# Performance work log

Hardware: AMD Instinct MI355X
Metric: run time of the kernel (lower is better)

## Reference

```python
import jax, jax.numpy as jnp
import numpy as np

D = 512
EPS = 1e-5  # torch BatchNorm1d default eps


def swish(x):
    return x * jax.nn.sigmoid(x)


def batchnorm_train(x, gamma, beta):
    # BatchNorm1d in training mode: biased batch stats
    m = jnp.mean(x, axis=0)
    v = jnp.mean((x - m) ** 2, axis=0)
    return gamma * (x - m) / jnp.sqrt(v + EPS) + beta


def setup_inputs() -> dict:
    key = jax.random.key(0)
    k_fea, k_w1, k_w2, k_lerp = jax.random.split(key, 4)
    bs, P = 32768, 8192
    fea = jax.random.normal(k_fea, (bs, D), dtype=jnp.float32)
    # first P rows are the minority (positive) class
    lbl = jnp.concatenate([jnp.ones((P, 1), jnp.int32), jnp.zeros((bs - P, 1), jnp.int32)], axis=0)
    scale = 1.0 / np.sqrt(D)
    W1 = jax.random.normal(k_w1, (D, D), dtype=jnp.float32) * scale
    W2 = jax.random.normal(k_w2, (D, D), dtype=jnp.float32) * scale
    b1 = jnp.zeros((D,), jnp.float32)
    b2 = jnp.zeros((D,), jnp.float32)
    g1 = jnp.ones((D,), jnp.float32)
    g2 = jnp.ones((D,), jnp.float32)
    beta1 = jnp.zeros((D,), jnp.float32)
    beta2 = jnp.zeros((D,), jnp.float32)
    lerp_w = jax.random.uniform(k_lerp, (P, 3), dtype=jnp.float32)
    return dict(fea=fea, lbl=lbl, W1=W1, b1=b1, g1=g1, beta1=beta1,
                W2=W2, b2=b2, g2=g2, beta2=beta2, lerp_w=lerp_w, num_pos=P)


def reference(fea, lbl, W1, b1, g1, beta1, W2, b2, g2, beta2, lerp_w, num_pos):
    # fea_transform: Linear -> BN -> Swish -> Linear -> BN -> Swish
    h = swish(batchnorm_train(fea @ W1 + b1, g1, beta1))
    h = swish(batchnorm_train(h @ W2 + b2, g2, beta2))

    # SMOTE path (training mode): KNN over positive-class features
    pos_idx = jnp.nonzero(lbl[:, 0] > 0, size=num_pos)[0]  # static-size gather
    x = h[pos_idx]                                          # (P, D)
    sq = jnp.sum(x * x, axis=-1)                            # (P,)
    # negative squared pairwise distance; topk largest == nearest
    neg_dist = 2.0 * (x @ x.T) - sq[:, None] - sq[None, :]  # (P, P)
    _, idx = jax.lax.top_k(neg_dist, 3)                     # (P, 3), idx[:,0] == self

    a = x[idx[:, 0]]                                        # (P, D) anchor
    b = x[idx]                                              # (P, 3, D) neighbors
    # torch.lerp(a, b, w) = a + w * (b - a), one random w per (i, j)
    new_fea = a[:, None, :] + lerp_w[..., None] * (b - a[:, None, :])
    new_fea = new_fea.reshape(-1, D)                        # (3P, D), row-major matches i,j loop order

    fea_out = jnp.concatenate([h, new_fea], axis=0)
    lbl_out = jnp.concatenate([lbl, jnp.ones((new_fea.shape[0], 1), lbl.dtype)], axis=0)
    return fea_out, lbl_out
```

## Files before the change

kernel.cpp:

```cpp
#include <hip/hip_runtime.h>
#include <math.h>

#define NEG_INF -3.402823466e38f
#define NSPLIT 16

typedef __attribute__((ext_vector_type(8))) short bf16x8;
typedef __attribute__((ext_vector_type(4))) float f32x4;

__device__ __forceinline__ void gload_lds16(const unsigned short* g, unsigned short* l) {
  __builtin_amdgcn_global_load_lds(
      (const __attribute__((address_space(1))) unsigned int*)g,
      (__attribute__((address_space(3))) unsigned int*)l, 16, 0, 0);
}
__device__ __forceinline__ void gload_lds16f(const float* g, float* l) {
  __builtin_amdgcn_global_load_lds(
      (const __attribute__((address_space(1))) unsigned int*)g,
      (__attribute__((address_space(3))) unsigned int*)l, 16, 0, 0);
}

__device__ __forceinline__ unsigned short f2bf(float f) {
  union { float f; unsigned int u; } a; a.f = f;
  unsigned int u = a.u;
  return (unsigned short)((u + 0x7fffu + ((u >> 16) & 1u)) >> 16);
}

__device__ __forceinline__ void split3_8(f32x4 a, f32x4 b,
                                         bf16x8& hi, bf16x8& md, bf16x8& lo) {
  union { bf16x8 v; unsigned int u[4]; } H, M, L;
  float f[8];
  f[0]=a[0]; f[1]=a[1]; f[2]=a[2]; f[3]=a[3];
  f[4]=b[0]; f[5]=b[1]; f[6]=b[2]; f[7]=b[3];
#pragma unroll
  for (int p = 0; p < 4; ++p) {
    union { float f; unsigned int u; } x0, x1, h0, h1, r0, r1, m0, m1, s0, s1;
    x0.f = f[2*p]; x1.f = f[2*p+1];
    H.u[p] = (x0.u >> 16) | (x1.u & 0xffff0000u);
    h0.u = x0.u & 0xffff0000u; h1.u = x1.u & 0xffff0000u;
    r0.f = x0.f - h0.f;        r1.f = x1.f - h1.f;
    M.u[p] = (r0.u >> 16) | (r1.u & 0xffff0000u);
    m0.u = r0.u & 0xffff0000u; m1.u = r1.u & 0xffff0000u;
    s0.f = r0.f - m0.f;        s1.f = r1.f - m1.f;
    L.u[p] = (s0.u >> 16) | (s1.u & 0xffff0000u);
  }
  hi = H.v; md = M.v; lo = L.v;
}

__global__ __launch_bounds__(256) void split_w_t3(const float* __restrict__ W,
    unsigned short* __restrict__ Th, unsigned short* __restrict__ Tm,
    unsigned short* __restrict__ Tl)
{
  __shared__ float T[64][65];
  int k0 = blockIdx.x * 64, n0 = blockIdx.y * 64;
  int tid = threadIdx.x;
  int r = tid >> 4, c4 = (tid & 15) << 2;
#pragma unroll
  for (int p = 0; p < 4; ++p) {
    int row = r + p * 16;
    float4 v = *(const float4*)&W[(size_t)(k0 + row) * 512 + n0 + c4];
    T[c4 + 0][row] = v.x; T[c4 + 1][row] = v.y;
    T[c4 + 2][row] = v.z; T[c4 + 3][row] = v.w;
  }
  __syncthreads();
  int nr = tid >> 2, kc = (tid & 3) << 4;
#pragma unroll
  for (int u = 0; u < 16; ++u) {
    union { float f; unsigned int u; } x, h, rr, m, ss;
    x.f = T[nr][kc + u];
    unsigned short hb = (unsigned short)(x.u >> 16);
    h.u = x.u & 0xffff0000u;
    rr.f = x.f - h.f;
    unsigned short mb = (unsigned short)(rr.u >> 16);
    m.u = rr.u & 0xffff0000u;
    ss.f = rr.f - m.f;
    unsigned short lb = (unsigned short)(ss.u >> 16);
    size_t o = (size_t)(n0 + nr) * 512 + k0 + kc + u;
    Th[o] = hb; Tm[o] = mb; Tl[o] = lb;
  }
}

__global__ __launch_bounds__(256, 2) void gemm_split3(
    const float* __restrict__ A, const unsigned short* __restrict__ Bth,
    const unsigned short* __restrict__ Btm, const unsigned short* __restrict__ Btl,
    const float* __restrict__ bias, float* __restrict__ C, float* __restrict__ partial)
{
  __shared__ char smem[81920];
  const int tid = threadIdx.x;
  const int w = tid >> 6, lane = tid & 63;
  const int wr = w >> 1, wc = w & 1;
  const int bm = blockIdx.x * 128, bn = blockIdx.y * 128;
  const int fr = lane & 15, fg = lane >> 4;
  const int arow = tid >> 3, acb = (tid & 7) << 4;
  const int brow = tid >> 2, bcb = (tid & 3) << 4;

  f32x4 acc[4][4];
#pragma unroll
  for (int mi = 0; mi < 4; ++mi)
#pragma unroll
    for (int ni = 0; ni < 4; ++ni) acc[mi][ni] = (f32x4){0.f, 0.f, 0.f, 0.f};

  auto STAGE = [&](int buf, int ktf) {
    float* sA = (float*)(smem + buf * 40960);
    unsigned short* sBh = (unsigned short*)(smem + buf * 40960 + 16384);
    unsigned short* sBm = sBh + 4096;
    unsigned short* sBl = sBm + 4096;
#pragma unroll
    for (int p = 0; p < 4; ++p) {
      int row = arow + p * 32;
      int cb = acb ^ ((row & 7) << 4);
      gload_lds16f(&A[(size_t)(bm + row) * 512 + ktf + (cb >> 2)],
                   &sA[row * 32 + (acb >> 2)]);
    }
#pragma unroll
    for (int p = 0; p < 2; ++p) {
      int row = brow + p * 64;
      int cb = bcb ^ (((row >> 1) & 3) << 4);
      int so = row * 32 + (bcb >> 1);
      gload_lds16(&Bth[(size_t)(bn + row) * 512 + ktf + (cb >> 1)], &sBh[so]);
      gload_lds16(&Btm[(size_t)(bn + row) * 512 + ktf + (cb >> 1)], &sBm[so]);
      gload_lds16(&Btl[(size_t)(bn + row) * 512 + ktf + (cb >> 1)], &sBl[so]);
    }
  };

  STAGE(0, 0);
  __syncthreads();
  for (int it = 0; it < 16; ++it) {
    int cur = it & 1;
    if (it + 1 < 16) STAGE(cur ^ 1, (it + 1) * 32);
    float* sA = (float*)(smem + cur * 40960);
    unsigned short* sBh = (unsigned short*)(smem + cur * 40960 + 16384);
    unsigned short* sBm = sBh + 4096;
    unsigned short* sBl = sBm + 4096;
    bf16x8 bh[4], bmf[4], blf[4];
#pragma unroll
    for (int ni = 0; ni < 4; ++ni) {
      int row = wc * 64 + ni * 16 + fr;
      int off = row * 32 + (((fg * 16) ^ (((row >> 1) & 3) << 4)) >> 1);
      bh[ni]  = *(const bf16x8*)&sBh[off];
      bmf[ni] = *(const bf16x8*)&sBm[off];
      blf[ni] = *(const bf16x8*)&sBl[off];
    }
    bf16x8 ah[4], am[4], al[4];
#pragma unroll
    for (int mi = 0; mi < 4; ++mi) {
      int row = wr * 64 + mi * 16 + fr;
      int swz = (row & 7) << 4;
      const char* rb = (const char*)(sA + row * 32);
      f32x4 f0 = *(const f32x4*)(rb + ((fg * 32) ^ swz));
      f32x4 f1 = *(const f32x4*)(rb + ((fg * 32 + 16) ^ swz));
      split3_8(f0, f1, ah[mi], am[mi], al[mi]);
    }
#pragma unroll
    for (int mi = 0; mi < 4; ++mi)
#pragma unroll
      for (int ni = 0; ni < 4; ++ni) {
        acc[mi][ni] = __builtin_amdgcn_mfma_f32_16x16x32_bf16(al[mi], bh[ni],  acc[mi][ni], 0, 0, 0);
        acc[mi][ni] = __builtin_amdgcn_mfma_f32_16x16x32_bf16(am[mi], bmf[ni], acc[mi][ni], 0, 0, 0);
        acc[mi][ni] = __builtin_amdgcn_mfma_f32_16x16x32_bf16(ah[mi], blf[ni], acc[mi][ni], 0, 0, 0);
        acc[mi][ni] = __builtin_amdgcn_mfma_f32_16x16x32_bf16(am[mi], bh[ni],  acc[mi][ni], 0, 0, 0);
        acc[mi][ni] = __builtin_amdgcn_mfma_f32_16x16x32_bf16(ah[mi], bmf[ni], acc[mi][ni], 0, 0, 0);
        acc[mi][ni] = __builtin_amdgcn_mfma_f32_16x16x32_bf16(ah[mi], bh[ni],  acc[mi][ni], 0, 0, 0);
      }
    __syncthreads();
  }
  float bno[4], s[4] = {0, 0, 0, 0}, q[4] = {0, 0, 0, 0};
#pragma unroll
  for (int ni = 0; ni < 4; ++ni) bno[ni] = bias[bn + wc * 64 + ni * 16 + fr];
#pragma unroll
  for (int mi = 0; mi < 4; ++mi) {
    int row = bm + wr * 64 + mi * 16 + fg * 4;
#pragma unroll
    for (int ni = 0; ni < 4; ++ni) {
      int col = bn + wc * 64 + ni * 16 + fr;
#pragma unroll
      for (int r = 0; r < 4; ++r) {
        float v = acc[mi][ni][r] + bno[ni];
        C[(size_t)(row + r) * 512 + col] = v;
        s[ni] += v; q[ni] += v * v;
      }
    }
  }
#pragma unroll
  for (int ni = 0; ni < 4; ++ni) {
    float ss = s[ni], qq = q[ni];
    ss += __shfl_xor(ss, 16); ss += __shfl_xor(ss, 32);
    qq += __shfl_xor(qq, 16); qq += __shfl_xor(qq, 32);
    if (fg == 0) {
      int slot = blockIdx.x * 2 + wr;
      int col = bn + wc * 64 + ni * 16 + fr;
      partial[(size_t)(slot * 2 + 0) * 512 + col] = ss;
      partial[(size_t)(slot * 2 + 1) * 512 + col] = qq;
    }
  }
}

__global__ __launch_bounds__(256) void bn_reduce1(
    const float* __restrict__ partial, float* __restrict__ partial2, int nslot)
{
  int g = blockIdx.x, p = blockIdx.y;
  int per = nslot >> 4;
  int t = threadIdx.x;
#pragma unroll
  for (int cc = 0; cc < 2; ++cc) {
    int c = t + cc * 256;
    float s = 0.f;
    for (int s0 = 0; s0 < per; ++s0) {
      int slot = g * per + s0;
      s += partial[(size_t)(slot * 2 + p) * 512 + c];
    }
    partial2[(size_t)(g * 2 + p) * 512 + c] = s;
  }
}

__global__ void bn_finalize(
    const float* __restrict__ partial2, const float* __restrict__ g,
    const float* __restrict__ beta, float* __restrict__ scale,
    float* __restrict__ shift, int rows)
{
  int c = blockIdx.x * blockDim.x + threadIdx.x;
  if (c >= 512) return;
  float s = 0, s2 = 0;
  for (int b = 0; b < 16; ++b) {
    s  += partial2[(size_t)(b * 2 + 0) * 512 + c];
    s2 += partial2[(size_t)(b * 2 + 1) * 512 + c];
  }
  float m = s / rows;
  float v = s2 / rows - m * m;
  if (v < 0) v = 0;
  float sc = g[c] / sqrtf(v + 1e-5f);
  scale[c] = sc;
  shift[c] = beta[c] - m * sc;
}

__global__ void bn_swish(
    const float* __restrict__ Y, const float* __restrict__ scale,
    const float* __restrict__ shift, float* __restrict__ H, int total4)
{
  int i = blockIdx.x * blockDim.x + threadIdx.x;
  if (i >= total4) return;
  float4 y = ((const float4*)Y)[i];
  int c = (i * 4) & 511;
  float z;
  float4 o;
  z = y.x * scale[c + 0] + shift[c + 0]; o.x = z / (1.f + expf(-z));
  z = y.y * scale[c + 1] + shift[c + 1]; o.y = z / (1.f + expf(-z));
  z = y.z * scale[c + 2] + shift[c + 2]; o.z = z / (1.f + expf(-z));
  z = y.w * scale[c + 3] + shift[c + 3]; o.w = z / (1.f + expf(-z));
  ((float4*)H)[i] = o;
}

__global__ __launch_bounds__(1024) void pos_count(const int* __restrict__ lbl, int n,
                                                  int* __restrict__ cnt,
                                                  int* __restrict__ pos, int P)
{
  int b = blockIdx.x, tid = threadIdx.x;
  int i = b * 1024 + tid;
  if (i < P) pos[i] = 0;
  int pred = (i < n) && (lbl[i] > 0);
  unsigned long long m = __ballot(pred);
  __shared__ int ws[16];
  if ((tid & 63) == 0) ws[tid >> 6] = __popcll(m);
  __syncthreads();
  if (tid == 0) { int s = 0; for (int k = 0; k < 16; ++k) s += ws[k]; cnt[b] = s; }
}

__global__ void pos_prefix(int* __restrict__ cnt, int nb)
{
  if (threadIdx.x == 0) {
    int s = 0;
    for (int b = 0; b < nb; ++b) { int c = cnt[b]; cnt[b] = s; s += c; }
  }
}

__global__ __launch_bounds__(1024) void pos_scatter(const int* __restrict__ lbl, int n,
                                                    const int* __restrict__ cntp,
                                                    int* __restrict__ pos, int P)
{
  int b = blockIdx.x, tid = threadIdx.x;
  int i = b * 1024 + tid;
  int pred = (i < n) && (lbl[i] > 0);
  unsigned long long m = __ballot(pred);
  __shared__ int ws[16];
  int wid = tid >> 6, lane = tid & 63;
  if (lane == 0) ws[wid] = __popcll(m);
  __syncthreads();
  int wbase = 0;
  for (int w2 = 0; w2 < wid; ++w2) wbase += ws[w2];
  int rank = cntp[b] + wbase + __popcll(m & ((1ull << lane) - 1ull));
  if (pred && rank < P) pos[rank] = i;
}

__global__ void gather_sq(const float* __restrict__ H, const int* __restrict__ pos,
                          float* __restrict__ X, unsigned short* __restrict__ Xh,
                          float* __restrict__ sq)
{
  int r = blockIdx.x, t = threadIdx.x;
  int src = pos[r];
  float4 v = *(const float4*)&H[src * 512 + t * 4];
  *(float4*)&X[r * 512 + t * 4] = v;
  ushort4 hv;
  hv.x = f2bf(v.x); hv.y = f2bf(v.y); hv.z = f2bf(v.z); hv.w = f2bf(v.w);
  *(ushort4*)&Xh[r * 512 + t * 4] = hv;
  float s = v.x * v.x + v.y * v.y + v.z * v.z + v.w * v.w;
#pragma unroll
  for (int off = 32; off > 0; off >>= 1) s += __shfl_down(s, off);
  __shared__ float red[2];
  if ((t & 63) == 0) red[t >> 6] = s;
  __syncthreads();
  if (t == 0) sq[r] = red[0] + red[1];
}

__global__ __launch_bounds__(256, 2) void gram8(
    const unsigned short* __restrict__ Xh, const float* __restrict__ sq, int P,
    float* __restrict__ p8v, int* __restrict__ p8j)
{
  __shared__ unsigned short Ah[128 * 64];
  __shared__ unsigned short Bh[128 * 64];
  __shared__ float dl[4][64][17];
  __shared__ float sqj_l[128];

  const int tid = threadIdx.x;
  const int w = tid >> 6, lane = tid & 63;
  const int wr = w >> 1, wc = w & 1;
  const int bi = blockIdx.x * 128;
  const int jchunk = P / NSPLIT;
  const int jlo = blockIdx.y * jchunk;

  const int srow = tid >> 3;
  const int scb  = (tid & 7) << 4;
  const int fr = lane & 15, fg = lane >> 4;

  float t[8]; int ji[8];
#pragma unroll
  for (int q = 0; q < 8; ++q) { t[q] = NEG_INF; ji[q] = 0x7fffffff; }

  for (int jt = 0; jt < jchunk; jt += 128) {
    const int j0 = jlo + jt;
    if (tid < 128) sqj_l[tid] = sq[j0 + tid];
    f32x4 acc[4][4];
#pragma unroll
    for (int mi = 0; mi < 4; ++mi)
#pragma unroll
      for (int ni = 0; ni < 4; ++ni) acc[mi][ni] = (f32x4){0.f, 0.f, 0.f, 0.f};

    for (int kt = 0; kt < 512; kt += 64) {
#pragma unroll
      for (int it = 0; it < 4; ++it) {
        int row = srow + it * 32;
        int cb = scb ^ ((row & 7) << 4);
        gload_lds16(&Xh[(size_t)(bi + row) * 512 + kt + (cb >> 1)],
                    &Ah[row * 64 + (scb >> 1)]);
        gload_lds16(&Xh[(size_t)(j0 + row) * 512 + kt + (cb >> 1)],
                    &Bh[row * 64 + (scb >> 1)]);
      }
      __syncthreads();
#pragma unroll
      for (int ks = 0; ks < 2; ++ks) {
        bf16x8 af[4], bfr[4];
        int kb = ks * 64 + fg * 16;
#pragma unroll
        for (int mi = 0; mi < 4; ++mi) {
          int row = wr * 64 + mi * 16 + fr;
          af[mi] = *(const bf16x8*)&Ah[row * 64 + ((kb ^ ((row & 7) << 4)) >> 1)];
        }
#pragma unroll
        for (int ni = 0; ni < 4; ++ni) {
          int row = wc * 64 + ni * 16 + fr;
          bfr[ni] = *(const bf16x8*)&Bh[row * 64 + ((kb ^ ((row & 7) << 4)) >> 1)];
        }
#pragma unroll
        for (int mi = 0; mi < 4; ++mi)
#pragma unroll
          for (int ni = 0; ni < 4; ++ni)
            acc[mi][ni] = __builtin_amdgcn_mfma_f32_16x16x32_bf16(
                af[mi], bfr[ni], acc[mi][ni], 0, 0, 0);
      }
      __syncthreads();
    }

#pragma unroll
    for (int qn = 0; qn < 4; ++qn) {
      float sqv = sqj_l[wc * 64 + qn * 16 + fr];
#pragma unroll
      for (int mi = 0; mi < 4; ++mi)
#pragma unroll
        for (int r = 0; r < 4; ++r)
          dl[w][mi * 16 + fg * 4 + r][fr] = 2.0f * acc[mi][qn][r] - sqv;
      __syncthreads();
      int jbase = j0 + wc * 64 + qn * 16;
      for (int c = 0; c < 16; ++c) {
        float v = dl[w][lane][c];
        if (v > t[7]) {
          t[7] = v; ji[7] = jbase + c;
#pragma unroll
          for (int q = 7; q > 0; --q) {
            if (t[q] > t[q - 1]) {
              float tv = t[q]; t[q] = t[q - 1]; t[q - 1] = tv;
              int tj = ji[q]; ji[q] = ji[q - 1]; ji[q - 1] = tj;
            }
          }
        }
      }
      __syncthreads();
    }
  }

  int row = bi + wr * 64 + lane;
  int set = blockIdx.y * 2 + wc;
  size_t base = ((size_t)row * (NSPLIT * 2) + set) * 8;
#pragma unroll
  for (int q = 0; q < 8; ++q) { p8v[base + q] = t[q]; p8j[base + q] = ji[q]; }
}

__global__ void merge8(const float* __restrict__ p8v, const int* __restrict__ p8j,
                       int* __restrict__ cand, int P)
{
  int i = blockIdx.x * blockDim.x + threadIdx.x;
  if (i >= P) return;
  const int S = NSPLIT * 2;
  int head[S];
#pragma unroll
  for (int s = 0; s < S; ++s) head[s] = 0;
  const float* v = p8v + (size_t)i * S * 8;
  const int* j = p8j + (size_t)i * S * 8;
  for (int k = 0; k < 8; ++k) {
    float bv = NEG_INF; int bj = 0x7fffffff; int bs = 0;
#pragma unroll
    for (int s = 0; s < S; ++s) {
      if (head[s] < 8) {
        float vv = v[s * 8 + head[s]];
        int jj = j[s * 8 + head[s]];
        if (vv > bv || (vv == bv && jj < bj)) { bv = vv; bj = jj; bs = s; }
      }
    }
    head[bs]++;
    cand[i * 8 + k] = bj;
  }
}

__global__ __launch_bounds__(64) void rescore(
    const float* __restrict__ X, const float* __restrict__ sq,
    const int* __restrict__ cand, int* __restrict__ idx3)
{
  int i = blockIdx.x;
  int lane = threadIdx.x;
  f32x4 x0 = *(const f32x4*)&X[(size_t)i * 512 + lane * 8];
  f32x4 x1 = *(const f32x4*)&X[(size_t)i * 512 + lane * 8 + 4];
  float d[8]; int cj[8];
#pragma unroll
  for (int c = 0; c < 8; ++c) {
    int j = cand[i * 8 + c];
    cj[c] = j;
    f32x4 y0 = *(const f32x4*)&X[(size_t)j * 512 + lane * 8];
    f32x4 y1 = *(const f32x4*)&X[(size_t)j * 512 + lane * 8 + 4];
    float p = x0.x * y0.x + x0.y * y0.y + x0.z * y0.z + x0.w * y0.w
            + x1.x * y1.x + x1.y * y1.y + x1.z * y1.z + x1.w * y1.w;
#pragma unroll
    for (int off = 32; off > 0; off >>= 1) p += __shfl_xor(p, off);
    d[c] = 2.0f * p - sq[i] - sq[j];
  }
  if (lane == 0) {
    for (int k = 0; k < 3; ++k) {
      int b = 0;
#pragma unroll
      for (int c = 1; c < 8; ++c)
        if (d[c] > d[b] || (d[c] == d[b] && cj[c] < cj[b])) b = c;
      idx3[i * 3 + k] = cj[b];
      d[b] = NEG_INF; cj[b] = 0x7fffffff;
    }
  }
}

__global__ void make_newfea(const float* __restrict__ X, const int* __restrict__ idx3,
                            const float* __restrict__ lw, float* __restrict__ out)
{
  int r = blockIdx.x;
  int i = r / 3, k = r - i * 3;
  int ai = idx3[i * 3 + 0];
  int bi = idx3[i * 3 + k];
  float w = lw[r];
  int t = threadIdx.x;
  float4 av = *(const float4*)&X[ai * 512 + t * 4];
  float4 bv = *(const float4*)&X[bi * 512 + t * 4];
  float4 o;
  o.x = av.x + w * (bv.x - av.x);
  o.y = av.y + w * (bv.y - av.y);
  o.z = av.z + w * (bv.z - av.z);
  o.w = av.w + w * (bv.w - av.w);
  *(float4*)&out[(size_t)r * 512 + t * 4] = o;
}

__global__ void write_lbl(const int* __restrict__ lbl, float* __restrict__ out,
                          int n_in, int n_total)
{
  int i = blockIdx.x * blockDim.x + threadIdx.x;
  if (i < n_total) out[i] = (i < n_in) ? (float)lbl[i] : 1.0f;
}

extern "C" void kernel_launch(void* const* d_in, const int* in_sizes, int n_in,
                              void* d_out, int out_size, void* d_ws, size_t ws_size,
                              hipStream_t stream)
{
  const float* fea   = (const float*)d_in[0];
  const int*   lbl   = (const int*)d_in[1];
  const float* W1    = (const float*)d_in[2];
  const float* b1    = (const float*)d_in[3];
  const float* g1    = (const float*)d_in[4];
  const float* beta1 = (const float*)d_in[5];
  const float* W2    = (const float*)d_in[6];
  const float* b2    = (const float*)d_in[7];
  const float* g2    = (const float*)d_in[8];
  const float* beta2 = (const float*)d_in[9];
  const float* lerp_w = (const float*)d_in[10];

  int bs = in_sizes[0] / 512;
  int P  = in_sizes[10] / 3;
  int n_total = bs + 3 * P;

  float* out_f = (float*)d_out;
  float* Hout = out_f;
  float* newfea = out_f + (size_t)bs * 512;
  float* lbl_out = out_f + (size_t)n_total * 512;

  const size_t MB = 1024 * 1024;
  const size_t KB = 1024;
  char* ws = (char*)d_ws;
  float* Y1 = (float*)ws;
  float* X  = (float*)(ws + 64 * MB);
  unsigned short* W1h = (unsigned short*)(ws + 64 * MB);
  unsigned short* W1m = (unsigned short*)(ws + 64 * MB + 512 * KB);
  unsigned short* W1l = (unsigned short*)(ws + 64 * MB + 1024 * KB);
  unsigned short* W2h = (unsigned short*)(ws + 64 * MB + 1536 * KB);
  unsigned short* W2m = (unsigned short*)(ws + 64 * MB + 2048 * KB);
  unsigned short* W2l = (unsigned short*)(ws + 64 * MB + 2560 * KB);
  float* partial = (float*)(ws + 80 * MB);
  float* scale = (float*)(ws + 82 * MB);
  float* shiftv = scale + 512;
  float* sq = shiftv + 512;
  int* pos = (int*)(sq + 8192);
  int* idx3 = pos + 8192;
  int* cnt = idx3 + 3 * 8192;
  float* partial2 = (float*)(ws + 83 * MB);
  unsigned short* Xh = (unsigned short*)ws;
  float* p8v = (float*)(ws + 8 * MB);
  int*   p8j = (int*)(ws + 16 * MB);
  int*   cand = (int*)(ws + 24 * MB);

  dim3 wgrid(8, 8);
  split_w_t3<<<wgrid, 256, 0, stream>>>(W1, W1h, W1m, W1l);
  split_w_t3<<<wgrid, 256, 0, stream>>>(W2, W2h, W2m, W2l);

  dim3 ggrid(bs / 128, 4);
  int nslot = (bs / 128) * 2;
  dim3 rgrid(16, 2);

  gemm_split3<<<ggrid, 256, 0, stream>>>(fea, W1h, W1m, W1l, b1, Y1, partial);
  bn_reduce1<<<rgrid, 256, 0, stream>>>(partial, partial2, nslot);
  bn_finalize<<<2, 256, 0, stream>>>(partial2, g1, beta1, scale, shiftv, bs);
  bn_swish<<<(bs * 512 / 4 + 255) / 256, 256, 0, stream>>>(Y1, scale, shiftv, Y1, bs * 512 / 4);

  gemm_split3<<<ggrid, 256, 0, stream>>>(Y1, W2h, W2m, W2l, b2, Hout, partial);
  bn_reduce1<<<rgrid, 256, 0, stream>>>(partial, partial2, nslot);
  bn_finalize<<<2, 256, 0, stream>>>(partial2, g2, beta2, scale, shiftv, bs);
  bn_swish<<<(bs * 512 / 4 + 255) / 256, 256, 0, stream>>>(Hout, scale, shiftv, Hout, bs * 512 / 4);

  int nb = (bs + 1023) / 1024;
  pos_count<<<nb, 1024, 0, stream>>>(lbl, bs, cnt, pos, P);
  pos_prefix<<<1, 64, 0, stream>>>(cnt, nb);
  pos_scatter<<<nb, 1024, 0, stream>>>(lbl, bs, cnt, pos, P);
  gather_sq<<<P, 128, 0, stream>>>(Hout, pos, X, Xh, sq);

  dim3 gram_grid(P / 128, NSPLIT);
  gram8<<<gram_grid, 256, 0, stream>>>(Xh, sq, P, p8v, p8j);
  merge8<<<(P + 255) / 256, 256, 0, stream>>>(p8v, p8j, cand, P);
  rescore<<<P, 64, 0, stream>>>(X, sq, cand, idx3);

  make_newfea<<<3 * P, 128, 0, stream>>>(X, idx3, lerp_w, newfea);
  write_lbl<<<(n_total + 255) / 256, 256, 0, stream>>>(lbl, lbl_out, bs, n_total);
}
```

Before: 529.7 us.

## Retile split3 GEMM warps, halve gram splits, and merge candidates wave-parallel

Result: faster. 465.2 us (-12.2%).

```diff
diff --git a/kernel.cpp b/kernel.cpp
--- a/kernel.cpp
+++ b/kernel.cpp
@@ -2,7 +2,7 @@
 #include <math.h>
 
 #define NEG_INF -3.402823466e38f
-#define NSPLIT 16
+#define NSPLIT 8
 
 typedef __attribute__((ext_vector_type(8))) short bf16x8;
 typedef __attribute__((ext_vector_type(4))) float f32x4;
@@ -86,17 +86,16 @@
   __shared__ char smem[81920];
   const int tid = threadIdx.x;
   const int w = tid >> 6, lane = tid & 63;
-  const int wr = w >> 1, wc = w & 1;
   const int bm = blockIdx.x * 128, bn = blockIdx.y * 128;
   const int fr = lane & 15, fg = lane >> 4;
   const int arow = tid >> 3, acb = (tid & 7) << 4;
   const int brow = tid >> 2, bcb = (tid & 3) << 4;
 
-  f32x4 acc[4][4];
-#pragma unroll
-  for (int mi = 0; mi < 4; ++mi)
-#pragma unroll
-    for (int ni = 0; ni < 4; ++ni) acc[mi][ni] = (f32x4){0.f, 0.f, 0.f, 0.f};
+  f32x4 acc[2][8];
+#pragma unroll
+  for (int mi = 0; mi < 2; ++mi)
+#pragma unroll
+    for (int ni = 0; ni < 8; ++ni) acc[mi][ni] = (f32x4){0.f, 0.f, 0.f, 0.f};
 
   auto STAGE = [&](int buf, int ktf) {
     float* sA = (float*)(smem + buf * 40960);
@@ -130,19 +129,10 @@
     unsigned short* sBh = (unsigned short*)(smem + cur * 40960 + 16384);
     unsigned short* sBm = sBh + 4096;
     unsigned short* sBl = sBm + 4096;
-    bf16x8 bh[4], bmf[4], blf[4];
-#pragma unroll
-    for (int ni = 0; ni < 4; ++ni) {
-      int row = wc * 64 + ni * 16 + fr;
-      int off = row * 32 + (((fg * 16) ^ (((row >> 1) & 3) << 4)) >> 1);
-      bh[ni]  = *(const bf16x8*)&sBh[off];
-      bmf[ni] = *(const bf16x8*)&sBm[off];
-      blf[ni] = *(const bf16x8*)&sBl[off];
-    }
-    bf16x8 ah[4], am[4], al[4];
-#pragma unroll
-    for (int mi = 0; mi < 4; ++mi) {
-      int row = wr * 64 + mi * 16 + fr;
+    bf16x8 ah[2], am[2], al[2];
+#pragma unroll
+    for (int mi = 0; mi < 2; ++mi) {
+      int row = w * 32 + mi * 16 + fr;
       int swz = (row & 7) << 4;
       const char* rb = (const char*)(sA + row * 32);
       f32x4 f0 = *(const f32x4*)(rb + ((fg * 32) ^ swz));
@@ -150,45 +140,66 @@
       split3_8(f0, f1, ah[mi], am[mi], al[mi]);
     }
 #pragma unroll
-    for (int mi = 0; mi < 4; ++mi)
-#pragma unroll
-      for (int ni = 0; ni < 4; ++ni) {
-        acc[mi][ni] = __builtin_amdgcn_mfma_f32_16x16x32_bf16(al[mi], bh[ni],  acc[mi][ni], 0, 0, 0);
-        acc[mi][ni] = __builtin_amdgcn_mfma_f32_16x16x32_bf16(am[mi], bmf[ni], acc[mi][ni], 0, 0, 0);
-        acc[mi][ni] = __builtin_amdgcn_mfma_f32_16x16x32_bf16(ah[mi], blf[ni], acc[mi][ni], 0, 0, 0);
-        acc[mi][ni] = __builtin_amdgcn_mfma_f32_16x16x32_bf16(am[mi], bh[ni],  acc[mi][ni], 0, 0, 0);
-        acc[mi][ni] = __builtin_amdgcn_mfma_f32_16x16x32_bf16(ah[mi], bmf[ni], acc[mi][ni], 0, 0, 0);
-        acc[mi][ni] = __builtin_amdgcn_mfma_f32_16x16x32_bf16(ah[mi], bh[ni],  acc[mi][ni], 0, 0, 0);
+    for (int ni = 0; ni < 8; ++ni) {
+      int row = ni * 16 + fr;
+      int off = row * 32 + (((fg * 16) ^ (((row >> 1) & 3) << 4)) >> 1);
+      bf16x8 bh  = *(const bf16x8*)&sBh[off];
+      bf16x8 bmf = *(const bf16x8*)&sBm[off];
+      bf16x8 blf = *(const bf16x8*)&sBl[off];
+#pragma unroll
+      for (int mi = 0; mi < 2; ++mi) {
+        acc[mi][ni] = __builtin_amdgcn_mfma_f32_16x16x32_bf16(al[mi], bh,  acc[mi][ni], 0, 0, 0);
+        acc[mi][ni] = __builtin_amdgcn_mfma_f32_16x16x32_bf16(am[mi], bmf, acc[mi][ni], 0, 0, 0);
+        acc[mi][ni] = __builtin_amdgcn_mfma_f32_16x16x32_bf16(ah[mi], blf, acc[mi][ni], 0, 0, 0);
+        acc[mi][ni] = __builtin_amdgcn_mfma_f32_16x16x32_bf16(am[mi], bh,  acc[mi][ni], 0, 0, 0);
+        acc[mi][ni] = __builtin_amdgcn_mfma_f32_16x16x32_bf16(ah[mi], bmf, acc[mi][ni], 0, 0, 0);
+        acc[mi][ni] = __builtin_amdgcn_mfma_f32_16x16x32_bf16(ah[mi], bh,  acc[mi][ni], 0, 0, 0);
       }
+    }
     __syncthreads();
   }
-  float bno[4], s[4] = {0, 0, 0, 0}, q[4] = {0, 0, 0, 0};
-#pragma unroll
-  for (int ni = 0; ni < 4; ++ni) bno[ni] = bias[bn + wc * 64 + ni * 16 + fr];
-#pragma unroll
-  for (int mi = 0; mi < 4; ++mi) {
-    int row = bm + wr * 64 + mi * 16 + fg * 4;
-#pragma unroll
-    for (int ni = 0; ni < 4; ++ni) {
-      int col = bn + wc * 64 + ni * 16 + fr;
+
+  float ssv[8], qqv[8];
+#pragma unroll
+  for (int ni = 0; ni < 8; ++ni) {
+    float bno = bias[bn + ni * 16 + fr];
+    float s = 0.f, q = 0.f;
+#pragma unroll
+    for (int mi = 0; mi < 2; ++mi) {
+      int row = bm + w * 32 + mi * 16 + fg * 4;
+      int col = bn + ni * 16 + fr;
 #pragma unroll
       for (int r = 0; r < 4; ++r) {
-        float v = acc[mi][ni][r] + bno[ni];
+        float v = acc[mi][ni][r] + bno;
         C[(size_t)(row + r) * 512 + col] = v;
-        s[ni] += v; q[ni] += v * v;
+        s += v; q += v * v;
       }
     }
-  }
-#pragma unroll
-  for (int ni = 0; ni < 4; ++ni) {
-    float ss = s[ni], qq = q[ni];
-    ss += __shfl_xor(ss, 16); ss += __shfl_xor(ss, 32);
-    qq += __shfl_xor(qq, 16); qq += __shfl_xor(qq, 32);
-    if (fg == 0) {
-      int slot = blockIdx.x * 2 + wr;
-      int col = bn + wc * 64 + ni * 16 + fr;
-      partial[(size_t)(slot * 2 + 0) * 512 + col] = ss;
-      partial[(size_t)(slot * 2 + 1) * 512 + col] = qq;
+    s += __shfl_xor(s, 16); s += __shfl_xor(s, 32);
+    q += __shfl_xor(q, 16); q += __shfl_xor(q, 32);
+    ssv[ni] = s; qqv[ni] = q;
+  }
+  float* ps = (float*)smem;
+  if (fg == 0) {
+#pragma unroll
+    for (int ni = 0; ni < 8; ++ni) {
+      ps[((w * 2 + 0) * 8 + ni) * 16 + fr] = ssv[ni];
+      ps[((w * 2 + 1) * 8 + ni) * 16 + fr] = qqv[ni];
+    }
+  }
+  __syncthreads();
+  if ((w & 1) == 0) {
+    int p = w >> 1;
+#pragma unroll
+    for (int k = 0; k < 4; ++k) {
+      int idx = k * 64 + lane;
+      int part = idx >> 7;
+      int rem = idx & 127;
+      int ni = rem >> 4, fr2 = rem & 15;
+      float v = ps[(((2 * p) * 2 + part) * 8 + ni) * 16 + fr2]
+              + ps[(((2 * p + 1) * 2 + part) * 8 + ni) * 16 + fr2];
+      int slot = blockIdx.x * 2 + p;
+      partial[(size_t)(slot * 2 + part) * 512 + bn + ni * 16 + fr2] = v;
     }
   }
 }
@@ -411,29 +422,30 @@
   for (int q = 0; q < 8; ++q) { p8v[base + q] = t[q]; p8j[base + q] = ji[q]; }
 }
 
-__global__ void merge8(const float* __restrict__ p8v, const int* __restrict__ p8j,
-                       int* __restrict__ cand, int P)
-{
-  int i = blockIdx.x * blockDim.x + threadIdx.x;
-  if (i >= P) return;
-  const int S = NSPLIT * 2;
-  int head[S];
-#pragma unroll
-  for (int s = 0; s < S; ++s) head[s] = 0;
-  const float* v = p8v + (size_t)i * S * 8;
-  const int* j = p8j + (size_t)i * S * 8;
+__global__ __launch_bounds__(256) void merge8w(const float* __restrict__ p8v,
+                                               const int* __restrict__ p8j,
+                                               int* __restrict__ cand, int P)
+{
+  int row = blockIdx.x * 4 + (threadIdx.x >> 6);
+  int lane = threadIdx.x & 63;
+  if (row >= P) return;
+  const float* v = p8v + (size_t)row * 128;
+  const int* j = p8j + (size_t)row * 128;
+  float v0 = v[lane * 2], v1 = v[lane * 2 + 1];
+  int j0 = j[lane * 2], j1 = j[lane * 2 + 1];
   for (int k = 0; k < 8; ++k) {
-    float bv = NEG_INF; int bj = 0x7fffffff; int bs = 0;
-#pragma unroll
-    for (int s = 0; s < S; ++s) {
-      if (head[s] < 8) {
-        float vv = v[s * 8 + head[s]];
-        int jj = j[s * 8 + head[s]];
-        if (vv > bv || (vv == bv && jj < bj)) { bv = vv; bj = jj; bs = s; }
-      }
-    }
-    head[bs]++;
-    cand[i * 8 + k] = bj;
+    float bv; int bj;
+    if (v0 > v1 || (v0 == v1 && j0 < j1)) { bv = v0; bj = j0; }
+    else { bv = v1; bj = j1; }
+#pragma unroll
+    for (int off = 1; off < 64; off <<= 1) {
+      float ov = __shfl_xor(bv, off);
+      int oj = __shfl_xor(bj, off);
+      if (ov > bv || (ov == bv && oj < bj)) { bv = ov; bj = oj; }
+    }
+    if (lane == 0) cand[row * 8 + k] = bj;
+    if (j0 == bj) { v0 = NEG_INF; j0 = 0x7fffffff; }
+    if (j1 == bj) { v1 = NEG_INF; j1 = 0x7fffffff; }
   }
 }
 
@@ -542,8 +554,8 @@
   float* partial2 = (float*)(ws + 83 * MB);
   unsigned short* Xh = (unsigned short*)ws;
   float* p8v = (float*)(ws + 8 * MB);
-  int*   p8j = (int*)(ws + 16 * MB);
-  int*   cand = (int*)(ws + 24 * MB);
+  int*   p8j = (int*)(ws + 12 * MB);
+  int*   cand = (int*)(ws + 16 * MB);
 
   dim3 wgrid(8, 8);
   split_w_t3<<<wgrid, 256, 0, stream>>>(W1, W1h, W1m, W1l);
@@ -571,7 +583,7 @@
 
   dim3 gram_grid(P / 128, NSPLIT);
   gram8<<<gram_grid, 256, 0, stream>>>(Xh, sq, P, p8v, p8j);
-  merge8<<<(P + 255) / 256, 256, 0, stream>>>(p8v, p8j, cand, P);
+  merge8w<<<(P + 3) / 4, 256, 0, stream>>>(p8v, p8j, cand, P);
   rescore<<<P, 64, 0, stream>>>(X, sq, cand, idx3);
 
   make_newfea<<<3 * P, 128, 0, stream>>>(X, idx3, lerp_w, newfea);
```
